# Performance work log

Hardware: AMD Instinct MI355X
Metric: run time of the kernel (lower is better)

## Reference

```python
import jax, jax.numpy as jnp
import numpy as np

N_HEADS = 4
LEAKY_SLOPE = 0.2


def setup_inputs() -> dict:
    key = jax.random.key(0)
    k1, k2, k3 = jax.random.split(key, 3)
    b, c, h, w = 8, 64, 128, 128
    z = jax.random.normal(k1, (b, c, h, w), dtype=jnp.float32)
    # torch.nn.Linear weights are (out_features, in_features); scale ~1/sqrt(fan_in)
    W_Q = jax.random.normal(k2, (c, c), dtype=jnp.float32) * 0.125
    W_K = jax.random.normal(k3, (c, c), dtype=jnp.float32) * 0.125
    return {"z": z, "W_Q": W_Q, "W_K": W_K}


def _axial_branch(z_perm_flat, z_raw_flat, W_Q, W_K, n_batch, seq, d_k, scale):
    # z_perm_flat: (n_batch, seq, c)  -- rearranged input fed to W_Q
    # z_raw_flat : (n_batch, seq, c)  -- raw memory-order reshape fed to W_K
    Q = jnp.matmul(z_perm_flat, W_Q.T).reshape(N_HEADS * n_batch, d_k, seq)
    V = jnp.matmul(z_raw_flat, W_K.T).reshape(N_HEADS * n_batch, d_k, seq)
    # QK-less scores: Q^T Q / sqrt(d_k)  -> (N, seq, seq)
    scores = jnp.einsum('nds,ndt->nst', Q, Q) * scale
    attn = jax.nn.softmax(scores, axis=-1)
    # right-multiply attention onto V, then LeakyReLU
    ctx = jnp.einsum('nds,nst->ndt', V, attn)
    return jax.nn.leaky_relu(ctx, negative_slope=LEAKY_SLOPE)


def reference(z, W_Q, W_K):
    b, c, h, w = z.shape
    d_k = c // N_HEADS
    scale = 1.0 / np.sqrt(d_k).astype(np.float32)

    # Branch 1 (attention over w): a = rearrange 'b c h w -> (b h) w c'
    a = jnp.transpose(z, (0, 2, 3, 1)).reshape(b * h, w, c)
    v1_in = z.reshape(b * h, w, c)  # raw reshape, as in the torch code
    context1 = _axial_branch(a, v1_in, W_Q, W_K, b * h, w, d_k, scale)

    # Branch 2 (attention over h): m = rearrange 'b c h w -> (b w) h c'
    m = jnp.transpose(z, (0, 3, 2, 1)).reshape(b * w, h, c)
    v2_in = z.reshape(b * w, h, c)  # raw reshape, as in the torch code
    context2 = _axial_branch(m, v2_in, W_Q, W_K, b * w, h, d_k, scale)

    context = context1 + context2  # requires h == w
    return context.reshape(b, c, h, w)
```

## Files before the change

### kernel.cpp

```cpp
#include <hip/hip_runtime.h>


typedef __attribute__((ext_vector_type(8))) short bh8;
typedef __attribute__((ext_vector_type(4))) float f32x4;
typedef unsigned short u16;
typedef unsigned int u32;

#define MFMA16(a,b,c) __builtin_amdgcn_mfma_f32_16x16x32_bf16(a,b,c,0,0,0)

#define AIMG_ST 72
#define QP_ST   40
#define VH_ST   136
#define PT_ST   136

#define OFF_AH   0
#define OFF_AL   4608
#define OFF_VIN  9216
#define OFF_PT   0
#define OFF_QP   34816
#define OFF_VH   45056
#define LDS_TOT  49408

__device__ __forceinline__ void split3(float f, u16& h, u16& l) {
    u32 u = __float_as_uint(f);
    u32 hf = u & 0xFFFF0000u;
    float r = f - __uint_as_float(hf);
    h = (u16)(hf >> 16);
    l = (u16)((__float_as_uint(r) + 0x8000u) >> 16);
}
__device__ __forceinline__ u16 rnbf(float f) {
    return (u16)((__float_as_uint(f) + 0x8000u) >> 16);
}
__device__ __forceinline__ u32 pkrn(float f0, float f1) {
    return ((__float_as_uint(f0) + 0x8000u) >> 16) |
           ((__float_as_uint(f1) + 0x8000u) & 0xFFFF0000u);
}
__device__ __forceinline__ float lrelu(float x) { return x > 0.f ? x : 0.2f * x; }

__global__ void split_w_kernel(const float* __restrict__ Wq,
                               const float* __restrict__ Wk,
                               u16* __restrict__ ws)
{
    const int i = blockIdx.x * 256 + threadIdx.x;
    const int j = i & 4095;
    const float f = (i < 4096) ? Wq[j] : Wk[j];
    const int base = (i < 4096) ? 0 : 8192;
    u16 h, l; split3(f, h, l);
    ws[base + j] = h;
    ws[base + 4096 + j] = l;
}

#define WOFF(n, ks) (((n)*16 + lid)*64 + (ks)*32 + quad*8)

__device__ __forceinline__ void gemm_q(const u16* Ah, const u16* Al,
                                       const u16* wsu,
                                       u16* qp, int miQ, int niA, int lid, int quad)
{
    const bh8 h0a = *(const bh8*)(wsu +        WOFF(niA+0,0));
    const bh8 h0b = *(const bh8*)(wsu +        WOFF(niA+0,1));
    const bh8 h1a = *(const bh8*)(wsu +        WOFF(niA+1,0));
    const bh8 h1b = *(const bh8*)(wsu +        WOFF(niA+1,1));
    const bh8 l0a = *(const bh8*)(wsu + 4096 + WOFF(niA+0,0));
    const bh8 l0b = *(const bh8*)(wsu + 4096 + WOFF(niA+0,1));
    const bh8 l1a = *(const bh8*)(wsu + 4096 + WOFF(niA+1,0));
    const bh8 l1b = *(const bh8*)(wsu + 4096 + WOFF(niA+1,1));
    const int offA = (miQ*16 + lid)*AIMG_ST + quad*8;
    bh8 ah0 = *(const bh8*)(Ah + offA);
    bh8 ah1 = *(const bh8*)(Ah + offA + 32);
    bh8 al0 = *(const bh8*)(Al + offA);
    bh8 al1 = *(const bh8*)(Al + offA + 32);
    f32x4 acc0 = {0.f,0.f,0.f,0.f}, acc1 = {0.f,0.f,0.f,0.f};
    acc0 = MFMA16(ah0, h0a, acc0); acc0 = MFMA16(ah0, l0a, acc0); acc0 = MFMA16(al0, h0a, acc0);
    acc0 = MFMA16(ah1, h0b, acc0); acc0 = MFMA16(ah1, l0b, acc0); acc0 = MFMA16(al1, h0b, acc0);
    acc1 = MFMA16(ah0, h1a, acc1); acc1 = MFMA16(ah0, l1a, acc1); acc1 = MFMA16(al0, h1a, acc1);
    acc1 = MFMA16(ah1, h1b, acc1); acc1 = MFMA16(ah1, l1b, acc1); acc1 = MFMA16(al1, h1b, acc1);
    #pragma unroll
    for (int r = 0; r < 4; ++r) {
        const int l = miQ*16 + quad*4 + r;
        const int d = l >> 1;
        const int sbase = (l & 1) << 6;
        u16 h, lo;
        const int s0 = sbase + (niA + 0)*16 + lid;
        split3(0.5f*acc0[r], h, lo);
        qp[s0*QP_ST + d] = h; qp[s0*QP_ST + 16 + d] = lo;
        const int s1 = sbase + (niA + 1)*16 + lid;
        split3(0.5f*acc1[r], h, lo);
        qp[s1*QP_ST + d] = h; qp[s1*QP_ST + 16 + d] = lo;
    }
}

__device__ __forceinline__ void gemm_v(const u16* Vin, const u16* wsu,
                                       u16* vh, int miQ, int niA, int lid, int quad)
{
    const bh8 h0a = *(const bh8*)(wsu + 8192 + WOFF(niA+0,0));
    const bh8 h0b = *(const bh8*)(wsu + 8192 + WOFF(niA+0,1));
    const bh8 h1a = *(const bh8*)(wsu + 8192 + WOFF(niA+1,0));
    const bh8 h1b = *(const bh8*)(wsu + 8192 + WOFF(niA+1,1));
    const int offA = (miQ*16 + lid)*AIMG_ST + quad*8;
    bh8 ah0 = *(const bh8*)(Vin + offA);
    bh8 ah1 = *(const bh8*)(Vin + offA + 32);
    f32x4 acc0 = {0.f,0.f,0.f,0.f}, acc1 = {0.f,0.f,0.f,0.f};
    acc0 = MFMA16(ah0, h0a, acc0); acc0 = MFMA16(ah1, h0b, acc0);
    acc1 = MFMA16(ah0, h1a, acc1); acc1 = MFMA16(ah1, h1b, acc1);
    #pragma unroll
    for (int r = 0; r < 4; ++r) {
        const int l = miQ*16 + quad*4 + r;
        const int d = l >> 1;
        const int sbase = (l & 1) << 6;
        vh[d*VH_ST + sbase + (niA + 0)*16 + lid] = rnbf(acc0[r]);
        vh[d*VH_ST + sbase + (niA + 1)*16 + lid] = rnbf(acc1[r]);
    }
}

__device__ __forceinline__ void gram_pt(const u16* Qp, u16* PT, int w, int lid, int quad)
{
    #pragma unroll
    for (int st = 0; st < 2; ++st) {
        const u16* arow = Qp + (32*w + st*16 + lid)*QP_ST;
        bh8 a1 = *(const bh8*)(arow + quad*8);
        bh8 t  = *(const bh8*)(arow + ((quad >= 2) ? (quad-2)*8 : 0));
        bh8 zz = t ^ t;
        bh8 a2 = (quad < 2) ? zz : t;
        f32x4 g[8];
        #pragma unroll
        for (int ti = 0; ti < 8; ++ti) {
            const u16* brow = Qp + (ti*16 + lid)*QP_ST;
            bh8 b1 = *(const bh8*)(brow + (quad & 1)*8);
            bh8 b2 = *(const bh8*)(brow + quad*8);
            f32x4 acc = {0.f,0.f,0.f,0.f};
            acc = MFMA16(a1, b1, acc);
            acc = MFMA16(a2, b2, acc);
            g[ti] = acc;
        }
        float inv[4];
        #pragma unroll
        for (int r = 0; r < 4; ++r) {
            float s = 0.f;
            #pragma unroll
            for (int ti = 0; ti < 8; ++ti) {
                const float p = __expf(g[ti][r]);
                g[ti][r] = p; s += p;
            }
            s += __shfl_xor(s, 1); s += __shfl_xor(s, 2);
            s += __shfl_xor(s, 4); s += __shfl_xor(s, 8);
            inv[r] = 1.0f / s;
        }
        const int col = 32*w + st*16 + quad*4;
        #pragma unroll
        for (int ti = 0; ti < 8; ++ti) {
            uint2 dv;
            dv.x = pkrn(g[ti][0]*inv[0], g[ti][1]*inv[1]);
            dv.y = pkrn(g[ti][2]*inv[2], g[ti][3]*inv[3]);
            *(uint2*)(PT + (ti*16 + lid)*PT_ST + col) = dv;
        }
    }
}

__device__ __forceinline__ void pv_ctx(const u16* PT, const u16* Vh,
                                       f32x4& c0, f32x4& c1, int w, int lid, int quad)
{
    #pragma unroll
    for (int tj2 = 0; tj2 < 2; ++tj2) {
        const int tj = 2*w + tj2;
        f32x4 acc = {0.f,0.f,0.f,0.f};
        #pragma unroll
        for (int ks = 0; ks < 4; ++ks) {
            bh8 pa = *(const bh8*)(PT + (tj*16 + lid)*PT_ST + ks*32 + quad*8);
            bh8 vb = *(const bh8*)(Vh + lid*VH_ST + ks*32 + quad*8);
            acc = MFMA16(pa, vb, acc);
        }
        if (tj2) c1 = acc; else c0 = acc;
    }
}

__global__ __launch_bounds__(256, 3)
void axial_attn_mfma(const float* __restrict__ z, const u16* __restrict__ wsu,
                     float* __restrict__ out)
{
    __shared__ __align__(16) unsigned char lds[LDS_TOT];
    u16* const ptAh = (u16*)(lds + OFF_AH);
    u16* const ptAl = (u16*)(lds + OFF_AL);
    u16* const ptPT = (u16*)(lds + OFF_PT);
    u16* const ptVI = (u16*)(lds + OFF_VIN);
    u16* const ptQP = (u16*)(lds + OFF_QP);
    u16* const ptVH = (u16*)(lds + OFF_VH);

    const int tid = threadIdx.x;
    const int w = tid >> 6, lane = tid & 63, quad = lane >> 4, lid = lane & 15;

    const int blk = blockIdx.x;
    const int j   = blk >> 3;
    const int xi  = ((blk & 7) << 4) | (j & 15);
    const int q   = (j >> 4) & 3;
    const int bi  = j >> 6;
    const int N   = (((bi << 7) | xi) << 2) | q;
    const size_t zbase = (size_t)bi << 20;

    const int ch0 = tid >> 5, l5 = tid & 31;
    const int vl0 = tid >> 4, vc0 = (tid & 15) << 2;
    const int miQ = w >> 1, niA = (w & 1) * 2;

    float a1r[8], a2r[8];
    float4 v4[2];
    {
        const float* s1 = z + zbase + ((size_t)xi << 7) + (q << 5) + l5;
        const float* s2 = z + zbase + (((size_t)(q*32 + l5)) << 7) + xi;
        #pragma unroll
        for (int k = 0; k < 8; ++k)
            a1r[k] = s1[(size_t)(ch0 + 8*k) << 14];
        const float4* sv = (const float4*)(z + ((size_t)N << 11));
        v4[0] = sv[tid]; v4[1] = sv[tid + 256];
        #pragma unroll
        for (int k = 0; k < 8; ++k)
            a2r[k] = s2[(size_t)(ch0 + 8*k) << 14];
    }

    #pragma unroll
    for (int k = 0; k < 8; ++k) {
        u16 h, lo; split3(a1r[k], h, lo);
        ptAh[l5*AIMG_ST + ch0 + 8*k] = h;
        ptAl[l5*AIMG_ST + ch0 + 8*k] = lo;
    }
    #pragma unroll
    for (int k = 0; k < 2; ++k) {
        const float4 vv = v4[k];
        uint2 dv;
        dv.x = pkrn(vv.x, vv.y);
        dv.y = pkrn(vv.z, vv.w);
        *(uint2*)(ptVI + (vl0 + 16*k)*AIMG_ST + vc0) = dv;
    }
    __syncthreads();

    gemm_q(ptAh, ptAl, wsu, ptQP, miQ, niA, lid, quad);
    gemm_v(ptVI, wsu, ptVH, miQ, niA, lid, quad);
    __syncthreads();

    gram_pt(ptQP, ptPT, w, lid, quad);
    __syncthreads();

    f32x4 c10, c11;
    pv_ctx(ptPT, ptVH, c10, c11, w, lid, quad);
    __syncthreads();

    #pragma unroll
    for (int k = 0; k < 8; ++k) {
        u16 h, lo; split3(a2r[k], h, lo);
        ptAh[l5*AIMG_ST + ch0 + 8*k] = h;
        ptAl[l5*AIMG_ST + ch0 + 8*k] = lo;
    }
    __syncthreads();

    gemm_q(ptAh, ptAl, wsu, ptQP, miQ, niA, lid, quad);
    __syncthreads();

    gram_pt(ptQP, ptPT, w, lid, quad);
    __syncthreads();

    f32x4 c20, c21;
    pv_ctx(ptPT, ptVH, c20, c21, w, lid, quad);

    float* ob = out + ((size_t)N << 11) + lid*128;
    #pragma unroll
    for (int tj2 = 0; tj2 < 2; ++tj2) {
        f32x4 a = tj2 ? c11 : c10;
        f32x4 b = tj2 ? c21 : c20;
        float4 ov;
        ov.x = lrelu(a[0]) + lrelu(b[0]);
        ov.y = lrelu(a[1]) + lrelu(b[1]);
        ov.z = lrelu(a[2]) + lrelu(b[2]);
        ov.w = lrelu(a[3]) + lrelu(b[3]);
        *(float4*)(ob + (2*w + tj2)*16 + quad*4) = ov;
    }
}

extern "C" void kernel_launch(void* const* d_in, const int* in_sizes, int n_in,
                              void* d_out, int out_size, void* d_ws, size_t ws_size,
                              hipStream_t stream) {
    const float* z  = (const float*)d_in[0];
    const float* Wq = (const float*)d_in[1];
    const float* Wk = (const float*)d_in[2];
    float* out = (float*)d_out;
    u16* ws = (u16*)d_ws;
    hipLaunchKernelGGL(split_w_kernel, dim3(32), dim3(256), 0, stream, Wq, Wk, ws);
    hipLaunchKernelGGL(axial_attn_mfma, dim3(4096), dim3(256), 0, stream, z, ws, out);
}
```

Baseline: 175.5 us.

## Split attention probability tile into two halves to shrink LDS and raise occupancy

The softmax probability matrix is now built and consumed in two 64-column halves, with the PV product accumulating across halves, instead of being stored whole. This halves the PT buffer stride and cuts total LDS per block, allowing launch bounds to target four blocks per CU instead of three. In exchange it adds two extra block-wide barriers per branch and a tighter register budget, which could cause spills.

```diff
diff --git a/kernel.cpp b/kernel.cpp
--- a/kernel.cpp
+++ b/kernel.cpp
@@ -11,15 +11,15 @@
 #define AIMG_ST 72
 #define QP_ST   40
 #define VH_ST   136
-#define PT_ST   136
+#define PT_ST   72
 
 #define OFF_AH   0
 #define OFF_AL   4608
 #define OFF_VIN  9216
 #define OFF_PT   0
-#define OFF_QP   34816
-#define OFF_VH   45056
-#define LDS_TOT  49408
+#define OFF_QP   18432
+#define OFF_VH   28672
+#define LDS_TOT  33024
 
 __device__ __forceinline__ void split3(float f, u16& h, u16& l) {
     u32 u = __float_as_uint(f);
@@ -112,68 +112,66 @@
     }
 }
 
-__device__ __forceinline__ void gram_pt(const u16* Qp, u16* PT, int w, int lid, int quad)
-{
-    #pragma unroll
-    for (int st = 0; st < 2; ++st) {
-        const u16* arow = Qp + (32*w + st*16 + lid)*QP_ST;
-        bh8 a1 = *(const bh8*)(arow + quad*8);
-        bh8 t  = *(const bh8*)(arow + ((quad >= 2) ? (quad-2)*8 : 0));
-        bh8 zz = t ^ t;
-        bh8 a2 = (quad < 2) ? zz : t;
-        f32x4 g[8];
+__device__ __forceinline__ void gram_pt(const u16* Qp, u16* PT, int h,
+                                        int w, int lid, int quad)
+{
+    const u16* arow = Qp + (h*64 + 16*w + lid)*QP_ST;
+    bh8 a1 = *(const bh8*)(arow + quad*8);
+    bh8 t  = *(const bh8*)(arow + ((quad >= 2) ? (quad-2)*8 : 0));
+    bh8 zz = t ^ t;
+    bh8 a2 = (quad < 2) ? zz : t;
+    f32x4 g[8];
+    #pragma unroll
+    for (int ti = 0; ti < 8; ++ti) {
+        const u16* brow = Qp + (ti*16 + lid)*QP_ST;
+        bh8 b1 = *(const bh8*)(brow + (quad & 1)*8);
+        bh8 b2 = *(const bh8*)(brow + quad*8);
+        f32x4 acc = {0.f,0.f,0.f,0.f};
+        acc = MFMA16(a1, b1, acc);
+        acc = MFMA16(a2, b2, acc);
+        g[ti] = acc;
+    }
+    float inv[4];
+    #pragma unroll
+    for (int r = 0; r < 4; ++r) {
+        float s = 0.f;
         #pragma unroll
         for (int ti = 0; ti < 8; ++ti) {
-            const u16* brow = Qp + (ti*16 + lid)*QP_ST;
-            bh8 b1 = *(const bh8*)(brow + (quad & 1)*8);
-            bh8 b2 = *(const bh8*)(brow + quad*8);
-            f32x4 acc = {0.f,0.f,0.f,0.f};
-            acc = MFMA16(a1, b1, acc);
-            acc = MFMA16(a2, b2, acc);
-            g[ti] = acc;
+            const float p = __expf(g[ti][r]);
+            g[ti][r] = p; s += p;
         }
-        float inv[4];
-        #pragma unroll
-        for (int r = 0; r < 4; ++r) {
-            float s = 0.f;
-            #pragma unroll
-            for (int ti = 0; ti < 8; ++ti) {
-                const float p = __expf(g[ti][r]);
-                g[ti][r] = p; s += p;
-            }
-            s += __shfl_xor(s, 1); s += __shfl_xor(s, 2);
-            s += __shfl_xor(s, 4); s += __shfl_xor(s, 8);
-            inv[r] = 1.0f / s;
-        }
-        const int col = 32*w + st*16 + quad*4;
-        #pragma unroll
-        for (int ti = 0; ti < 8; ++ti) {
-            uint2 dv;
-            dv.x = pkrn(g[ti][0]*inv[0], g[ti][1]*inv[1]);
-            dv.y = pkrn(g[ti][2]*inv[2], g[ti][3]*inv[3]);
-            *(uint2*)(PT + (ti*16 + lid)*PT_ST + col) = dv;
-        }
-    }
-}
-
-__device__ __forceinline__ void pv_ctx(const u16* PT, const u16* Vh,
+        s += __shfl_xor(s, 1); s += __shfl_xor(s, 2);
+        s += __shfl_xor(s, 4); s += __shfl_xor(s, 8);
+        inv[r] = 1.0f / s;
+    }
+    const int col = 16*w + quad*4;
+    #pragma unroll
+    for (int ti = 0; ti < 8; ++ti) {
+        uint2 dv;
+        dv.x = pkrn(g[ti][0]*inv[0], g[ti][1]*inv[1]);
+        dv.y = pkrn(g[ti][2]*inv[2], g[ti][3]*inv[3]);
+        *(uint2*)(PT + (ti*16 + lid)*PT_ST + col) = dv;
+    }
+}
+
+__device__ __forceinline__ void pv_ctx(const u16* PT, const u16* Vh, int h,
                                        f32x4& c0, f32x4& c1, int w, int lid, int quad)
 {
     #pragma unroll
     for (int tj2 = 0; tj2 < 2; ++tj2) {
         const int tj = 2*w + tj2;
-        f32x4 acc = {0.f,0.f,0.f,0.f};
-        #pragma unroll
-        for (int ks = 0; ks < 4; ++ks) {
+        f32x4 acc = tj2 ? c1 : c0;
+        #pragma unroll
+        for (int ks = 0; ks < 2; ++ks) {
             bh8 pa = *(const bh8*)(PT + (tj*16 + lid)*PT_ST + ks*32 + quad*8);
-            bh8 vb = *(const bh8*)(Vh + lid*VH_ST + ks*32 + quad*8);
+            bh8 vb = *(const bh8*)(Vh + lid*VH_ST + h*64 + ks*32 + quad*8);
             acc = MFMA16(pa, vb, acc);
         }
         if (tj2) c1 = acc; else c0 = acc;
     }
 }
 
-__global__ __launch_bounds__(256, 3)
+__global__ __launch_bounds__(256, 4)
 void axial_attn_mfma(const float* __restrict__ z, const u16* __restrict__ wsu,
                      float* __restrict__ out)
 {
@@ -235,11 +233,14 @@
     gemm_v(ptVI, wsu, ptVH, miQ, niA, lid, quad);
     __syncthreads();
 
-    gram_pt(ptQP, ptPT, w, lid, quad);
-    __syncthreads();
-
-    f32x4 c10, c11;
-    pv_ctx(ptPT, ptVH, c10, c11, w, lid, quad);
+    f32x4 c10 = {0.f,0.f,0.f,0.f}, c11 = {0.f,0.f,0.f,0.f};
+    gram_pt(ptQP, ptPT, 0, w, lid, quad);
+    __syncthreads();
+    pv_ctx(ptPT, ptVH, 0, c10, c11, w, lid, quad);
+    __syncthreads();
+    gram_pt(ptQP, ptPT, 1, w, lid, quad);
+    __syncthreads();
+    pv_ctx(ptPT, ptVH, 1, c10, c11, w, lid, quad);
     __syncthreads();
 
     #pragma unroll
@@ -253,11 +254,14 @@
     gemm_q(ptAh, ptAl, wsu, ptQP, miQ, niA, lid, quad);
     __syncthreads();
 
-    gram_pt(ptQP, ptPT, w, lid, quad);
-    __syncthreads();
-
-    f32x4 c20, c21;
-    pv_ctx(ptPT, ptVH, c20, c21, w, lid, quad);
+    f32x4 c20 = {0.f,0.f,0.f,0.f}, c21 = {0.f,0.f,0.f,0.f};
+    gram_pt(ptQP, ptPT, 0, w, lid, quad);
+    __syncthreads();
+    pv_ctx(ptPT, ptVH, 0, c20, c21, w, lid, quad);
+    __syncthreads();
+    gram_pt(ptQP, ptPT, 1, w, lid, quad);
+    __syncthreads();
+    pv_ctx(ptPT, ptVH, 1, c20, c21, w, lid, quad);
 
     float* ob = out + ((size_t)N << 11) + lid*128;
     #pragma unroll
```

Result: faster. 162.5 us (-7.4%).
